# Performance work log

Measured on AMD Instinct MI355X. Metric: run time of the kernel, lower is better.

## Reference

```python
import jax, jax.numpy as jnp
import numpy as np

T_STEPS = 4
LAYERS = 10
CYCLE = 10
C = 64
TAU = 1.2
V_TH = 0.5
SG_ALPHA = 4.0  # spikingjelly default surrogate.Sigmoid alpha


@jax.custom_vjp
def heaviside_sg(x):
    return (x >= 0.0).astype(x.dtype)

def _h_fwd(x):
    return heaviside_sg(x), x

def _h_bwd(x, g):
    s = jax.nn.sigmoid(SG_ALPHA * x)
    return (SG_ALPHA * s * (1.0 - s) * g,)

heaviside_sg.defvjp(_h_fwd, _h_bwd)


def lif(x_seq):
    # MultiStepLIFNode: v' = v + (x - (v - v_reset))/tau, hard reset to v_reset=0,
    # detach_reset=True -> spike in reset path is stop-gradient'ed.
    def step(v, x):
        v = v + (x - v) / TAU
        spike = heaviside_sg(v - V_TH)
        v = v * (1.0 - jax.lax.stop_gradient(spike))
        return v, spike
    _, spikes = jax.lax.scan(step, jnp.zeros_like(x_seq[0]), x_seq)
    return spikes


def conv_seq(x, w, b, dilation=1):
    # x: [T,B,Cin,L]; w: [Cout,Cin,K]; 'same' padding for odd K
    T, B, Ci, L = x.shape
    K = w.shape[-1]
    pad = (K - 1) * dilation // 2
    y = jax.lax.conv_general_dilated(
        x.reshape(T * B, Ci, L), w, (1,), [(pad, pad)],
        rhs_dilation=(dilation,), dimension_numbers=('NCH', 'OIH', 'NCH'))
    y = y + b[None, :, None]
    return y.reshape(T, B, -1, L)


def setup_inputs() -> dict:
    key = jax.random.key(0)
    ks = jax.random.split(key, 20)
    B, L = 4, 4096
    s = 0.1
    n = jax.random.normal
    inp = {
        'audio': jax.random.uniform(ks[0], (B, L), dtype=jnp.float32),
        'diffusion_step': jax.random.randint(ks[1], (B,), 0, 50),
        'W_in': n(ks[2], (C, 1, 1), jnp.float32) * s,
        'b_in': n(ks[3], (C,), jnp.float32) * s,
        'demb_w1': n(ks[4], (LAYERS, C, 1), jnp.float32) * s,
        'demb_b1': n(ks[5], (LAYERS, C), jnp.float32) * s,
        'demb_w2': n(ks[6], (LAYERS, C, C), jnp.float32) * s,
        'demb_b2': n(ks[7], (LAYERS, C), jnp.float32) * s,
        'dproj_w': n(ks[8], (LAYERS, C, C), jnp.float32) * s,
        'dproj_b': n(ks[9], (LAYERS, C), jnp.float32) * s,
        'conv_w': n(ks[10], (LAYERS, 2 * C, C, 3), jnp.float32) * 0.05,
        'conv_b': n(ks[11], (LAYERS, 2 * C), jnp.float32) * s,
        'skip_w': n(ks[12], (LAYERS, C, C, 1), jnp.float32) * s,
        'skip_b': n(ks[13], (LAYERS, C), jnp.float32) * s,
        'res_w': n(ks[14], (LAYERS, C, C, 1), jnp.float32) * s,
        'res_b': n(ks[15], (LAYERS, C), jnp.float32) * s,
        'W_out': n(ks[16], (1, C, 1), jnp.float32) * s,
        'b_out': n(ks[17], (1,), jnp.float32) * s,
    }
    return inp


def reference(audio, diffusion_step, W_in, b_in, demb_w1, demb_b1, demb_w2,
              demb_b2, dproj_w, dproj_b, conv_w, conv_b, skip_w, skip_b,
              res_w, res_b, W_out, b_out):
    B, L = audio.shape
    # Poisson encoder: spike = 1[u < x] per timestep (fixed key -> deterministic)
    u = jax.random.uniform(jax.random.key(42), (T_STEPS, B, 1, L), dtype=jnp.float32)
    spike_seq = (u < audio[None, :, None, :]).astype(jnp.float32)

    x = conv_seq(spike_seq, W_in, b_in)          # [T,B,C,L]
    x = lif(x)

    d = diffusion_step.astype(jnp.float32)[:, None]  # [B,1]
    total_skip = jnp.zeros_like(x)
    for i in range(LAYERS):
        dilation = 2 ** (i % CYCLE)
        emb = jax.nn.silu(d @ demb_w1[i].T + demb_b1[i]) @ demb_w2[i].T + demb_b2[i]  # [B,C]
        proj = emb @ dproj_w[i].T + dproj_b[i]                                        # [B,C]
        y = x + proj[None, :, :, None]
        y = conv_seq(y, conv_w[i], conv_b[i], dilation=dilation)  # [T,B,2C,L]
        y = lif(y)
        gate, filt = jnp.split(y, 2, axis=2)
        y = jax.nn.sigmoid(gate) * jnp.tanh(filt)
        total_skip = total_skip + conv_seq(y, skip_w[i], skip_b[i])
        x = x + conv_seq(y, res_w[i], res_b[i])

    total_skip = jax.nn.relu(total_skip)
    out = conv_seq(total_skip, W_out, b_out)  # [T,B,1,L]
    out = lif(out)
    return out.sum(axis=0)  # [B,1,L]
```

## Files before the change

### kernel.cpp

```cpp
#include <hip/hip_runtime.h>

#define LL 4096
#define NB 4
#define NC 64
#define NT 4
#define NLAYERS 10
#define XS 5120
#define XPAD 512

typedef float v2f __attribute__((ext_vector_type(2)));

__device__ __forceinline__ void threefry2x32(unsigned x0, unsigned x1,
                                             unsigned& o0, unsigned& o1) {
  const unsigned ks0 = 0u, ks1 = 42u;
  const unsigned ks2 = 0x1BD11BDAu ^ ks0 ^ ks1;
  const unsigned ks[3] = {ks0, ks1, ks2};
  const unsigned r0[4] = {13u, 15u, 26u, 6u};
  const unsigned r1[4] = {17u, 29u, 16u, 24u};
  x0 += ks0; x1 += ks1;
#pragma unroll
  for (int g = 0; g < 5; ++g) {
    const unsigned* rr = (g & 1) ? r1 : r0;
#pragma unroll
    for (int j = 0; j < 4; ++j) {
      x0 += x1;
      unsigned r = rr[j];
      x1 = (x1 << r) | (x1 >> (32u - r));
      x1 ^= x0;
    }
    x0 += ks[(g + 1) % 3];
    x1 += ks[(g + 2) % 3] + (unsigned)(g + 1);
  }
  o0 = x0; o1 = x1;
}

__device__ __forceinline__ float u01(unsigned bits) {
  return __uint_as_float((bits >> 9) | 0x3f800000u) - 1.0f;
}

__device__ __forceinline__ float lif_step(float& v, float xt) {
  v = v + (xt - v) / 1.2f;
  float s = (v >= 0.5f) ? 1.0f : 0.0f;
  v = v * (1.0f - s);
  return s;
}

__global__ void prep_kernel(const float* __restrict__ skip_w,
                            const float* __restrict__ res_w,
                            const float* __restrict__ conv_w,
                            float* __restrict__ skipT,
                            float* __restrict__ resT,
                            float* __restrict__ wT) {
  int i = blockIdx.x;
  for (int idx = threadIdx.x; idx < 4096; idx += 256) {
    int c = idx >> 6, cp = idx & 63;
    skipT[i * 4096 + cp * 64 + c] = skip_w[i * 4096 + c * 64 + cp];
    resT[i * 4096 + cp * 64 + c] = res_w[i * 4096 + c * 64 + cp];
  }
  for (int idx = threadIdx.x; idx < 8 * 64 * 3 * 16; idx += 256) {
    int col = idx & 15;
    int r = idx >> 4;
    int k = r % 3; r /= 3;
    int ci = r % 64;
    int g = r / 64;
    int co = (col < 8) ? (g * 8 + col) : (64 + g * 8 + (col - 8));
    wT[i * 24576 + idx] = conv_w[(i * 128 + co) * 192 + ci * 3 + k];
  }
}

__global__ void proj_kernel(const int* __restrict__ dstep,
                            const float* __restrict__ w1, const float* __restrict__ b1,
                            const float* __restrict__ w2, const float* __restrict__ b2,
                            const float* __restrict__ pw, const float* __restrict__ pb,
                            float* __restrict__ proj) {
  __shared__ float e1[NB][NC];
  __shared__ float e2[NB][NC];
  int i = blockIdx.x;
  int tid = threadIdx.x;
  int b = tid >> 6, c = tid & 63;
  float d = (float)dstep[b];
  float v = d * w1[i * 64 + c] + b1[i * 64 + c];
  v = v / (1.0f + expf(-v));
  e1[b][c] = v;
  __syncthreads();
  float a = b2[i * 64 + c];
  for (int cp = 0; cp < 64; ++cp) a += e1[b][cp] * w2[(i * 64 + c) * 64 + cp];
  e2[b][c] = a;
  __syncthreads();
  float p = pb[i * 64 + c];
  for (int cp = 0; cp < 64; ++cp) p += e2[b][cp] * pw[(i * 64 + c) * 64 + cp];
  proj[(i * 4 + b) * 64 + c] = p;
}

__global__ void pc_kernel(const float* __restrict__ proj,
                          const float* __restrict__ conv_w,
                          float* __restrict__ pc) {
  __shared__ float pv[64];
  int layer = blockIdx.x, b = blockIdx.y;
  int tid = threadIdx.x;
  if (tid < 64) pv[tid] = proj[(layer * 4 + b) * 64 + tid];
  __syncthreads();
  int co = tid;
  const float* w = conv_w + (layer * 128 + co) * 192;
  float s0 = 0.0f, s1 = 0.0f, s2 = 0.0f;
  for (int ci = 0; ci < 64; ++ci) {
    float p = pv[ci];
    s0 += p * w[ci * 3 + 0];
    s1 += p * w[ci * 3 + 1];
    s2 += p * w[ci * 3 + 2];
  }
  float* o = pc + ((layer * 4 + b) * 128 + co) * 3;
  o[0] = s0; o[1] = s1; o[2] = s2;
}

__global__ void padzero_kernel(float* __restrict__ x) {
  int row = blockIdx.x;
  float* base = x + (size_t)row * XS;
  for (int i = threadIdx.x; i < XPAD; i += 256) {
    base[i] = 0.0f;
    base[XPAD + LL + i] = 0.0f;
  }
}

__global__ void encode_lif_kernel(const float* __restrict__ audio,
                                  const float* __restrict__ W_in,
                                  const float* __restrict__ b_in,
                                  float* __restrict__ x) {
  int tid = threadIdx.x;
  int lq = tid & 63, grp = tid >> 6;
  int l = blockIdx.x * 64 + lq;
  int b = blockIdx.y;
  float a = audio[b * LL + l];
  unsigned p0 = (unsigned)(b * LL + l);
  unsigned p1 = 16384u + p0;
  unsigned o00, o01, o10, o11;
  threefry2x32(p0, p0 + 32768u, o00, o01);
  threefry2x32(p1, p1 + 32768u, o10, o11);
  float sp[4];
  sp[0] = (u01(o00) < a) ? 1.0f : 0.0f;
  sp[1] = (u01(o10) < a) ? 1.0f : 0.0f;
  sp[2] = (u01(o01) < a) ? 1.0f : 0.0f;
  sp[3] = (u01(o11) < a) ? 1.0f : 0.0f;
  for (int j = 0; j < 16; ++j) {
    int c = grp * 16 + j;
    float w = W_in[c], bb = b_in[c];
    float v = 0.0f;
#pragma unroll
    for (int t = 0; t < 4; ++t) {
      float s = lif_step(v, w * sp[t] + bb);
      x[(size_t)((t * 4 + b) * 64 + c) * XS + XPAD + l] = s;
    }
  }
}

template <int DIL>
__global__ __launch_bounds__(256) void layer_conv_kernel(
    const float* __restrict__ x, const float* __restrict__ wT,
    const float* __restrict__ conv_b, const float* __restrict__ pc,
    float* __restrict__ y, int layer) {
  __shared__ float wg_lds[192 * 8];
  int tid = threadIdx.x;
  int g = blockIdx.y;
  int b = blockIdx.z;
  int l = blockIdx.x * 256 + tid;
  const float* wbase = wT + (size_t)(layer * 8 + g) * 3072;

  for (int idx = tid; idx < 1536; idx += 256) {
    wg_lds[idx] = wbase[(idx >> 3) * 16 + (idx & 7)];
  }
  __syncthreads();

  const float* px[4];
#pragma unroll
  for (int t = 0; t < 4; ++t)
    px[t] = x + (size_t)((t * 4 + b) * 64) * XS + XPAD + l;

  v2f ag[16], af[16];
#pragma unroll
  for (int q = 0; q < 16; ++q) {
    ag[q] = (v2f)(0.0f);
    af[q] = (v2f)(0.0f);
  }

  float xa[12], xb[12];
  auto loadx = [&](float* dst) {
#pragma unroll
    for (int t = 0; t < 4; ++t) {
      dst[t * 3 + 0] = px[t][-DIL];
      dst[t * 3 + 1] = px[t][0];
      dst[t * 3 + 2] = px[t][DIL];
      px[t] += XS;
    }
  };
  auto compute = [&](int ci, const float* xv) {
#pragma unroll
    for (int k = 0; k < 3; ++k) {
      const v2f* gw = (const v2f*)&wg_lds[(ci * 3 + k) * 8];
      const v2f* fw = (const v2f*)&wbase[(ci * 3 + k) * 16 + 8];
      v2f g0 = gw[0], g1 = gw[1], g2 = gw[2], g3 = gw[3];
      v2f f0 = fw[0], f1 = fw[1], f2 = fw[2], f3 = fw[3];
#pragma unroll
      for (int t = 0; t < 4; ++t) {
        float xq = xv[t * 3 + k];
        v2f x2;
        x2.x = xq; x2.y = xq;
        ag[t * 4 + 0] += g0 * x2;
        ag[t * 4 + 1] += g1 * x2;
        ag[t * 4 + 2] += g2 * x2;
        ag[t * 4 + 3] += g3 * x2;
        af[t * 4 + 0] += f0 * x2;
        af[t * 4 + 1] += f1 * x2;
        af[t * 4 + 2] += f2 * x2;
        af[t * 4 + 3] += f3 * x2;
      }
    }
  };

  loadx(xa);
  for (int ci = 0; ci < 64; ci += 2) {
    loadx(xb);
    compute(ci, xa);
    if (ci + 2 < 64) loadx(xa);
    compute(ci + 1, xb);
  }

  const float SIG1 = 0.73105857863000489f;
  const float TANH1 = 0.76159415595576486f;
  bool lb = (l < DIL), rb = (l >= LL - DIL);
#pragma unroll
  for (int j = 0; j < 8; ++j) {
    int cog = g * 8 + j;
    int cof = 64 + g * 8 + j;
    const float* pg = pc + ((layer * 4 + b) * 128 + cog) * 3;
    const float* pf = pc + ((layer * 4 + b) * 128 + cof) * 3;
    float S0g = pg[0], S1g = pg[1], S2g = pg[2];
    float S0f = pf[0], S1f = pf[1], S2f = pf[2];
    float bg = conv_b[layer * 128 + cog] + S0g + S1g + S2g;
    float bf = conv_b[layer * 128 + cof] + S0f + S1f + S2f;
    bg -= (lb ? S0g : 0.0f) + (rb ? S2g : 0.0f);
    bf -= (lb ? S0f : 0.0f) + (rb ? S2f : 0.0f);
    float vg = 0.0f, vf = 0.0f;
#pragma unroll
    for (int t = 0; t < 4; ++t) {
      float av = ag[t * 4 + (j >> 1)][j & 1];
      float fv = af[t * 4 + (j >> 1)][j & 1];
      float sg = lif_step(vg, av + bg);
      float sf = lif_step(vf, fv + bf);
      float gv = (sg != 0.0f) ? SIG1 : 0.5f;
      float tv = (sf != 0.0f) ? TANH1 : 0.0f;
      y[(size_t)((t * 4 + b) * 64 + cog) * LL + l] = gv * tv;
    }
  }
}

__global__ __launch_bounds__(256) void skip_res_kernel(
    const float* __restrict__ y, const float* __restrict__ skipT,
    const float* __restrict__ resT, const float* __restrict__ skip_b,
    const float* __restrict__ res_b, float* __restrict__ tskip,
    float* __restrict__ x, int layer) {
  int tid = threadIdx.x;
  int lg = tid & 31;
  int cg = tid >> 5;
  int cv = blockIdx.y;
  int tb = blockIdx.z;
  int l0 = blockIdx.x * 256 + lg * 8;
  int c0 = cg * 8;

  const float* wsrc = (cv ? resT : skipT) + layer * 4096 + c0;
  const float* yb = y + (size_t)tb * 64 * LL + l0;

  v2f acc[32];
#pragma unroll
  for (int q = 0; q < 32; ++q) acc[q] = (v2f)(0.0f);

  float4 w0a = *(const float4*)&wsrc[0];
  float4 w1a = *(const float4*)&wsrc[4];
  float4 y0a = *(const float4*)&yb[0];
  float4 y1a = *(const float4*)&yb[4];

  for (int cp = 0; cp < 64; ++cp) {
    int cpn = (cp < 63) ? cp + 1 : 63;
    float4 w0b = *(const float4*)&wsrc[cpn * 64];
    float4 w1b = *(const float4*)&wsrc[cpn * 64 + 4];
    float4 y0b = *(const float4*)&yb[(size_t)cpn * LL];
    float4 y1b = *(const float4*)&yb[(size_t)cpn * LL + 4];

    float wv[8] = {w0a.x, w0a.y, w0a.z, w0a.w, w1a.x, w1a.y, w1a.z, w1a.w};
    v2f yv[4];
    yv[0].x = y0a.x; yv[0].y = y0a.y;
    yv[1].x = y0a.z; yv[1].y = y0a.w;
    yv[2].x = y1a.x; yv[2].y = y1a.y;
    yv[3].x = y1a.z; yv[3].y = y1a.w;
#pragma unroll
    for (int i = 0; i < 8; ++i) {
      v2f w2;
      w2.x = wv[i]; w2.y = wv[i];
      acc[i * 4 + 0] += w2 * yv[0];
      acc[i * 4 + 1] += w2 * yv[1];
      acc[i * 4 + 2] += w2 * yv[2];
      acc[i * 4 + 3] += w2 * yv[3];
    }
    w0a = w0b; w1a = w1b; y0a = y0b; y1a = y1b;
  }

  const float* bsrc = (cv ? res_b : skip_b) + layer * 64 + c0;
#pragma unroll
  for (int i = 0; i < 8; ++i) {
    float bb = bsrc[i];
    float r[8];
#pragma unroll
    for (int j = 0; j < 8; ++j) r[j] = acc[i * 4 + (j >> 1)][j & 1] + bb;
    if (cv == 0) {
      size_t idx = (size_t)(tb * 64 + c0 + i) * LL + l0;
      float4 o0, o1;
      if (layer == 0) {
        o0.x = o0.y = o0.z = o0.w = 0.0f;
        o1 = o0;
      } else {
        o0 = *(const float4*)&tskip[idx];
        o1 = *(const float4*)&tskip[idx + 4];
      }
      o0.x += r[0]; o0.y += r[1]; o0.z += r[2]; o0.w += r[3];
      o1.x += r[4]; o1.y += r[5]; o1.z += r[6]; o1.w += r[7];
      *(float4*)&tskip[idx] = o0;
      *(float4*)&tskip[idx + 4] = o1;
    } else {
      size_t idx = (size_t)(tb * 64 + c0 + i) * XS + XPAD + l0;
      float4 o0 = *(const float4*)&x[idx];
      float4 o1 = *(const float4*)&x[idx + 4];
      o0.x += r[0]; o0.y += r[1]; o0.z += r[2]; o0.w += r[3];
      o1.x += r[4]; o1.y += r[5]; o1.z += r[6]; o1.w += r[7];
      *(float4*)&x[idx] = o0;
      *(float4*)&x[idx + 4] = o1;
    }
  }
}

__global__ void out_kernel(const float* __restrict__ tskip,
                           const float* __restrict__ W_out,
                           const float* __restrict__ b_out,
                           float* __restrict__ out) {
  __shared__ float red[4][4][64];
  int tid = threadIdx.x;
  int lq = tid & 63, grp = tid >> 6;
  int l = blockIdx.x * 64 + lq;
  int b = blockIdx.y;
  float acc[4] = {0.0f, 0.0f, 0.0f, 0.0f};
  for (int j = 0; j < 16; ++j) {
    int c = grp * 16 + j;
    float w = W_out[c];
#pragma unroll
    for (int t = 0; t < 4; ++t) {
      float sv = tskip[(size_t)((t * 4 + b) * 64 + c) * LL + l];
      acc[t] += fmaxf(sv, 0.0f) * w;
    }
  }
#pragma unroll
  for (int t = 0; t < 4; ++t) red[grp][t][lq] = acc[t];
  __syncthreads();
  if (grp == 0) {
    float bo = b_out[0];
    float v = 0.0f, s = 0.0f;
#pragma unroll
    for (int t = 0; t < 4; ++t) {
      float a = red[0][t][lq] + red[1][t][lq] + red[2][t][lq] + red[3][t][lq] + bo;
      s += lif_step(v, a);
    }
    out[b * LL + l] = s;
  }
}

extern "C" void kernel_launch(void* const* d_in, const int* in_sizes, int n_in,
                              void* d_out, int out_size, void* d_ws, size_t ws_size,
                              hipStream_t stream) {
  const float* audio   = (const float*)d_in[0];
  const int*   dstep   = (const int*)d_in[1];
  const float* W_in    = (const float*)d_in[2];
  const float* b_in    = (const float*)d_in[3];
  const float* demb_w1 = (const float*)d_in[4];
  const float* demb_b1 = (const float*)d_in[5];
  const float* demb_w2 = (const float*)d_in[6];
  const float* demb_b2 = (const float*)d_in[7];
  const float* dproj_w = (const float*)d_in[8];
  const float* dproj_b = (const float*)d_in[9];
  const float* conv_w  = (const float*)d_in[10];
  const float* conv_b  = (const float*)d_in[11];
  const float* skip_w  = (const float*)d_in[12];
  const float* skip_b  = (const float*)d_in[13];
  const float* res_w   = (const float*)d_in[14];
  const float* res_b   = (const float*)d_in[15];
  const float* W_out   = (const float*)d_in[16];
  const float* b_out   = (const float*)d_in[17];
  float* out = (float*)d_out;
  float* ws = (float*)d_ws;

  float* proj  = ws;
  float* skipT = proj + 2560;
  float* resT  = skipT + 40960;
  float* pc    = resT + 40960;
  float* wT    = pc + 15360;
  float* x     = wT + 245760;
  float* y     = x + 5242880;
  float* tskip = y + 4194304;

  prep_kernel<<<10, 256, 0, stream>>>(skip_w, res_w, conv_w, skipT, resT, wT);
  proj_kernel<<<10, 256, 0, stream>>>(dstep, demb_w1, demb_b1, demb_w2, demb_b2,
                                      dproj_w, dproj_b, proj);
  pc_kernel<<<dim3(10, 4), 128, 0, stream>>>(proj, conv_w, pc);
  padzero_kernel<<<1024, 256, 0, stream>>>(x);
  encode_lif_kernel<<<dim3(64, 4), 256, 0, stream>>>(audio, W_in, b_in, x);

  for (int i = 0; i < NLAYERS; ++i) {
    dim3 gc(16, 8, 4);
    switch (i) {
      case 0: layer_conv_kernel<1><<<gc, 256, 0, stream>>>(x, wT, conv_b, pc, y, i); break;
      case 1: layer_conv_kernel<2><<<gc, 256, 0, stream>>>(x, wT, conv_b, pc, y, i); break;
      case 2: layer_conv_kernel<4><<<gc, 256, 0, stream>>>(x, wT, conv_b, pc, y, i); break;
      case 3: layer_conv_kernel<8><<<gc, 256, 0, stream>>>(x, wT, conv_b, pc, y, i); break;
      case 4: layer_conv_kernel<16><<<gc, 256, 0, stream>>>(x, wT, conv_b, pc, y, i); break;
      case 5: layer_conv_kernel<32><<<gc, 256, 0, stream>>>(x, wT, conv_b, pc, y, i); break;
      case 6: layer_conv_kernel<64><<<gc, 256, 0, stream>>>(x, wT, conv_b, pc, y, i); break;
      case 7: layer_conv_kernel<128><<<gc, 256, 0, stream>>>(x, wT, conv_b, pc, y, i); break;
      case 8: layer_conv_kernel<256><<<gc, 256, 0, stream>>>(x, wT, conv_b, pc, y, i); break;
      case 9: layer_conv_kernel<512><<<gc, 256, 0, stream>>>(x, wT, conv_b, pc, y, i); break;
    }
    skip_res_kernel<<<dim3(16, 2, 16), 256, 0, stream>>>(y, skipT, resT, skip_b,
                                                         res_b, tskip, x, i);
  }
  out_kernel<<<dim3(64, 4), 256, 0, stream>>>(tskip, W_out, b_out, out);
}
```

Baseline: 854.7 us.

## Interleave timesteps innermost in activation buffers for float4 accesses

Changes the x, y and tskip buffers from [T,B,C,L] to [B,C,L,T], so the four timesteps of one position sit together. The conv, skip/res, encode and output kernels now load and store one float4 per position instead of four strided scalars. The skip/res grid is reshaped so each thread covers 2 positions × 4 timesteps. This cuts the number of memory instructions and address computations. The cost is that each conv thread reads 16 bytes per tap, and dilated neighbours are now 4x farther apart in memory.

Result: no change. 838.2 us (-1.9%).

```diff
diff --git a/kernel.cpp b/kernel.cpp
--- a/kernel.cpp
+++ b/kernel.cpp
@@ -115,10 +115,10 @@
 
 __global__ void padzero_kernel(float* __restrict__ x) {
   int row = blockIdx.x;
-  float* base = x + (size_t)row * XS;
+  float* base = x + (size_t)row * XS * 4;
   for (int i = threadIdx.x; i < XPAD; i += 256) {
-    base[i] = 0.0f;
-    base[XPAD + LL + i] = 0.0f;
+    *(float4*)&base[i * 4] = float4{0.f, 0.f, 0.f, 0.f};
+    *(float4*)&base[(XPAD + LL + i) * 4] = float4{0.f, 0.f, 0.f, 0.f};
   }
 }
 
@@ -145,11 +145,11 @@
     int c = grp * 16 + j;
     float w = W_in[c], bb = b_in[c];
     float v = 0.0f;
-#pragma unroll
-    for (int t = 0; t < 4; ++t) {
-      float s = lif_step(v, w * sp[t] + bb);
-      x[(size_t)((t * 4 + b) * 64 + c) * XS + XPAD + l] = s;
-    }
+    float4 o;
+    float* op = (float*)&o;
+#pragma unroll
+    for (int t = 0; t < 4; ++t) op[t] = lif_step(v, w * sp[t] + bb);
+    *(float4*)&x[(size_t)((b * 64 + c) * XS + XPAD + l) * 4] = o;
   }
 }
 
@@ -170,10 +170,7 @@
   }
   __syncthreads();
 
-  const float* px[4];
-#pragma unroll
-  for (int t = 0; t < 4; ++t)
-    px[t] = x + (size_t)((t * 4 + b) * 64) * XS + XPAD + l;
+  const float* px = x + (size_t)(b * 64 * XS + XPAD + l) * 4;
 
   v2f ag[16], af[16];
 #pragma unroll
@@ -182,26 +179,24 @@
     af[q] = (v2f)(0.0f);
   }
 
-  float xa[12], xb[12];
-  auto loadx = [&](float* dst) {
-#pragma unroll
-    for (int t = 0; t < 4; ++t) {
-      dst[t * 3 + 0] = px[t][-DIL];
-      dst[t * 3 + 1] = px[t][0];
-      dst[t * 3 + 2] = px[t][DIL];
-      px[t] += XS;
-    }
+  float4 xa[3], xb[3];
+  auto loadx = [&](float4* dst) {
+    dst[0] = *(const float4*)(px - (size_t)DIL * 4);
+    dst[1] = *(const float4*)px;
+    dst[2] = *(const float4*)(px + (size_t)DIL * 4);
+    px += (size_t)XS * 4;
   };
-  auto compute = [&](int ci, const float* xv) {
+  auto compute = [&](int ci, const float4* xv) {
 #pragma unroll
     for (int k = 0; k < 3; ++k) {
       const v2f* gw = (const v2f*)&wg_lds[(ci * 3 + k) * 8];
       const v2f* fw = (const v2f*)&wbase[(ci * 3 + k) * 16 + 8];
       v2f g0 = gw[0], g1 = gw[1], g2 = gw[2], g3 = gw[3];
       v2f f0 = fw[0], f1 = fw[1], f2 = fw[2], f3 = fw[3];
+      const float* xk = (const float*)&xv[k];
 #pragma unroll
       for (int t = 0; t < 4; ++t) {
-        float xq = xv[t * 3 + k];
+        float xq = xk[t];
         v2f x2;
         x2.x = xq; x2.y = xq;
         ag[t * 4 + 0] += g0 * x2;
@@ -240,6 +235,8 @@
     bg -= (lb ? S0g : 0.0f) + (rb ? S2g : 0.0f);
     bf -= (lb ? S0f : 0.0f) + (rb ? S2f : 0.0f);
     float vg = 0.0f, vf = 0.0f;
+    float4 o;
+    float* op = (float*)&o;
 #pragma unroll
     for (int t = 0; t < 4; ++t) {
       float av = ag[t * 4 + (j >> 1)][j & 1];
@@ -248,8 +245,9 @@
       float sf = lif_step(vf, fv + bf);
       float gv = (sg != 0.0f) ? SIG1 : 0.5f;
       float tv = (sf != 0.0f) ? TANH1 : 0.0f;
-      y[(size_t)((t * 4 + b) * 64 + cog) * LL + l] = gv * tv;
-    }
+      op[t] = gv * tv;
+    }
+    *(float4*)&y[(size_t)((b * 64 + cog) * LL + l) * 4] = o;
   }
 }
 
@@ -262,12 +260,12 @@
   int lg = tid & 31;
   int cg = tid >> 5;
   int cv = blockIdx.y;
-  int tb = blockIdx.z;
-  int l0 = blockIdx.x * 256 + lg * 8;
+  int b = blockIdx.z;
+  int l0 = blockIdx.x * 64 + lg * 2;
   int c0 = cg * 8;
 
   const float* wsrc = (cv ? resT : skipT) + layer * 4096 + c0;
-  const float* yb = y + (size_t)tb * 64 * LL + l0;
+  const float* yb = y + (size_t)(b * 64 * LL + l0) * 4;
 
   v2f acc[32];
 #pragma unroll
@@ -275,30 +273,27 @@
 
   float4 w0a = *(const float4*)&wsrc[0];
   float4 w1a = *(const float4*)&wsrc[4];
-  float4 y0a = *(const float4*)&yb[0];
-  float4 y1a = *(const float4*)&yb[4];
+  float4 y0a = *(const float4*)yb;
+  float4 y1a = *(const float4*)(yb + 4);
 
   for (int cp = 0; cp < 64; ++cp) {
     int cpn = (cp < 63) ? cp + 1 : 63;
     float4 w0b = *(const float4*)&wsrc[cpn * 64];
     float4 w1b = *(const float4*)&wsrc[cpn * 64 + 4];
-    float4 y0b = *(const float4*)&yb[(size_t)cpn * LL];
-    float4 y1b = *(const float4*)&yb[(size_t)cpn * LL + 4];
+    float4 y0b = *(const float4*)(yb + (size_t)cpn * LL * 4);
+    float4 y1b = *(const float4*)(yb + (size_t)cpn * LL * 4 + 4);
 
     float wv[8] = {w0a.x, w0a.y, w0a.z, w0a.w, w1a.x, w1a.y, w1a.z, w1a.w};
-    v2f yv[4];
-    yv[0].x = y0a.x; yv[0].y = y0a.y;
-    yv[1].x = y0a.z; yv[1].y = y0a.w;
-    yv[2].x = y1a.x; yv[2].y = y1a.y;
-    yv[3].x = y1a.z; yv[3].y = y1a.w;
+    const v2f* yp0 = (const v2f*)&y0a;
+    const v2f* yp1 = (const v2f*)&y1a;
 #pragma unroll
     for (int i = 0; i < 8; ++i) {
       v2f w2;
       w2.x = wv[i]; w2.y = wv[i];
-      acc[i * 4 + 0] += w2 * yv[0];
-      acc[i * 4 + 1] += w2 * yv[1];
-      acc[i * 4 + 2] += w2 * yv[2];
-      acc[i * 4 + 3] += w2 * yv[3];
+      acc[i * 4 + 0] += w2 * yp0[0];
+      acc[i * 4 + 1] += w2 * yp0[1];
+      acc[i * 4 + 2] += w2 * yp1[0];
+      acc[i * 4 + 3] += w2 * yp1[1];
     }
     w0a = w0b; w1a = w1b; y0a = y0b; y1a = y1b;
   }
@@ -309,12 +304,15 @@
     float bb = bsrc[i];
     float r[8];
 #pragma unroll
-    for (int j = 0; j < 8; ++j) r[j] = acc[i * 4 + (j >> 1)][j & 1] + bb;
+    for (int q = 0; q < 4; ++q) {
+      r[q * 2 + 0] = acc[i * 4 + q][0] + bb;
+      r[q * 2 + 1] = acc[i * 4 + q][1] + bb;
+    }
     if (cv == 0) {
-      size_t idx = (size_t)(tb * 64 + c0 + i) * LL + l0;
+      size_t idx = (size_t)((b * 64 + c0 + i) * LL + l0) * 4;
       float4 o0, o1;
       if (layer == 0) {
-        o0.x = o0.y = o0.z = o0.w = 0.0f;
+        o0 = float4{0.f, 0.f, 0.f, 0.f};
         o1 = o0;
       } else {
         o0 = *(const float4*)&tskip[idx];
@@ -325,7 +323,7 @@
       *(float4*)&tskip[idx] = o0;
       *(float4*)&tskip[idx + 4] = o1;
     } else {
-      size_t idx = (size_t)(tb * 64 + c0 + i) * XS + XPAD + l0;
+      size_t idx = (size_t)((b * 64 + c0 + i) * XS + XPAD + l0) * 4;
       float4 o0 = *(const float4*)&x[idx];
       float4 o1 = *(const float4*)&x[idx + 4];
       o0.x += r[0]; o0.y += r[1]; o0.z += r[2]; o0.w += r[3];
@@ -349,11 +347,11 @@
   for (int j = 0; j < 16; ++j) {
     int c = grp * 16 + j;
     float w = W_out[c];
-#pragma unroll
-    for (int t = 0; t < 4; ++t) {
-      float sv = tskip[(size_t)((t * 4 + b) * 64 + c) * LL + l];
-      acc[t] += fmaxf(sv, 0.0f) * w;
-    }
+    float4 sv = *(const float4*)&tskip[(size_t)((b * 64 + c) * LL + l) * 4];
+    acc[0] += fmaxf(sv.x, 0.0f) * w;
+    acc[1] += fmaxf(sv.y, 0.0f) * w;
+    acc[2] += fmaxf(sv.z, 0.0f) * w;
+    acc[3] += fmaxf(sv.w, 0.0f) * w;
   }
 #pragma unroll
   for (int t = 0; t < 4; ++t) red[grp][t][lq] = acc[t];
@@ -407,7 +405,7 @@
   proj_kernel<<<10, 256, 0, stream>>>(dstep, demb_w1, demb_b1, demb_w2, demb_b2,
                                       dproj_w, dproj_b, proj);
   pc_kernel<<<dim3(10, 4), 128, 0, stream>>>(proj, conv_w, pc);
-  padzero_kernel<<<1024, 256, 0, stream>>>(x);
+  padzero_kernel<<<256, 256, 0, stream>>>(x);
   encode_lif_kernel<<<dim3(64, 4), 256, 0, stream>>>(audio, W_in, b_in, x);
 
   for (int i = 0; i < NLAYERS; ++i) {
@@ -424,8 +422,8 @@
       case 8: layer_conv_kernel<256><<<gc, 256, 0, stream>>>(x, wT, conv_b, pc, y, i); break;
       case 9: layer_conv_kernel<512><<<gc, 256, 0, stream>>>(x, wT, conv_b, pc, y, i); break;
     }
-    skip_res_kernel<<<dim3(16, 2, 16), 256, 0, stream>>>(y, skipT, resT, skip_b,
-                                                         res_b, tskip, x, i);
+    skip_res_kernel<<<dim3(64, 2, 4), 256, 0, stream>>>(y, skipT, resT, skip_b,
+                                                        res_b, tskip, x, i);
   }
   out_kernel<<<dim3(64, 4), 256, 0, stream>>>(tskip, W_out, b_out, out);
 }
```
